# Performance work log

Hardware: AMD Instinct MI355X
Metric: run time of the kernel (lower is better)

The kernel has to match this reference:

```python
import jax, jax.numpy as jnp
import numpy as np

D_MODEL = 64
NODES = 325
TOPK = 8
HEADS = 4
D_INNER = 2 * D_MODEL      # mamba_ssm default expand=2
D_STATE = 16               # mamba_ssm default
D_CONV = 4                 # mamba_ssm default
DT_RANK = 4                # ceil(d_model/16)
B_SZ, T_LEN = 8, 64
EPS = 1e-5


def _layernorm(x, g, b):
    m = jnp.mean(x, -1, keepdims=True)
    v = jnp.mean(jnp.square(x - m), -1, keepdims=True)
    return (x - m) * jax.lax.rsqrt(v + EPS) * g + b


def _mamba(h, in_proj_w, conv_w, conv_b, x_proj_w, dt_w, dt_b, A_log, D_ssm, out_w):
    # h: (BN, T, D_MODEL)
    BN, T, _ = h.shape
    xz = h @ in_proj_w.T                      # (BN,T,2*di)
    xi, z = jnp.split(xz, 2, axis=-1)
    # depthwise causal conv1d, kernel D_CONV (unrolled: tiny fixed loop)
    xp = jnp.pad(xi, ((0, 0), (D_CONV - 1, 0), (0, 0)))
    xc = conv_b + sum(xp[:, j:j + T, :] * conv_w[:, j] for j in range(D_CONV))
    xc = jax.nn.silu(xc)
    dbl = xc @ x_proj_w.T                     # (BN,T,dt_rank+2*ds)
    dt = dbl[..., :DT_RANK]
    Bc = dbl[..., DT_RANK:DT_RANK + D_STATE]
    Cc = dbl[..., DT_RANK + D_STATE:]
    dt = jax.nn.softplus(dt @ dt_w.T + dt_b)  # (BN,T,di)
    A = -jnp.exp(A_log)                       # (di,ds)

    def step(hs, inp):
        dt_t, B_t, C_t, x_t = inp             # (BN,di),(BN,ds),(BN,ds),(BN,di)
        dA = jnp.exp(dt_t[..., None] * A)     # (BN,di,ds)
        hs = hs * dA + (dt_t * x_t)[..., None] * B_t[:, None, :]
        y = jnp.einsum('bds,bs->bd', hs, C_t)
        return hs, y

    tm = lambda a: jnp.swapaxes(a, 0, 1)      # time-major for scan
    h0 = jnp.zeros((BN, D_INNER, D_STATE), xc.dtype)
    _, ys = jax.lax.scan(step, h0, (tm(dt), tm(Bc), tm(Cc), tm(xc)))
    y = tm(ys) + D_ssm * xc
    y = y * jax.nn.silu(z)
    return y @ out_w.T


def setup_inputs() -> dict:
    key = jax.random.key(0)
    ks = jax.random.split(key, 24)
    rn = lambda k, s, sc=0.05: jax.random.normal(k, s, jnp.float32) * sc
    inp = {}
    inp['x'] = jax.random.normal(ks[0], (B_SZ, T_LEN, NODES, D_MODEL), jnp.float32)
    adj = jax.random.normal(ks[1], (NODES, NODES), jnp.float32)
    _, nbr = jax.lax.top_k(adj, TOPK)
    inp['neighbor_idx'] = nbr.astype(jnp.int32)           # (N, k) static buffer
    # temporal block
    inp['ln1_g'] = jnp.ones((D_MODEL,)); inp['ln1_b'] = jnp.zeros((D_MODEL,))
    inp['in_proj_w'] = rn(ks[2], (2 * D_INNER, D_MODEL))
    inp['conv_w'] = rn(ks[3], (D_INNER, D_CONV), 0.2)
    inp['conv_b'] = jnp.zeros((D_INNER,))
    inp['x_proj_w'] = rn(ks[4], (DT_RANK + 2 * D_STATE, D_INNER))
    inp['dt_w'] = rn(ks[5], (D_INNER, DT_RANK), 0.5)
    inp['dt_b'] = rn(ks[6], (D_INNER,), 0.5)
    inp['A_log'] = jnp.log(jnp.tile(jnp.arange(1, D_STATE + 1, dtype=jnp.float32), (D_INNER, 1)))
    inp['D_ssm'] = jnp.ones((D_INNER,))
    inp['out_w'] = rn(ks[7], (D_MODEL, D_INNER))
    # sparse graph attention
    for nm, k in (('q', 8), ('k', 9), ('v', 10), ('o', 11)):
        inp[nm + '_w'] = rn(ks[k], (D_MODEL, D_MODEL))
        inp[nm + '_b'] = jnp.zeros((D_MODEL,))
    # adaptive gate (final bias init -2.0 per module)
    inp['g1_w'] = rn(ks[12], (D_MODEL // 4, D_MODEL))
    inp['g1_b'] = jnp.zeros((D_MODEL // 4,))
    inp['g2_w'] = rn(ks[13], (1, D_MODEL // 4))
    inp['g2_b'] = jnp.full((1,), -2.0, jnp.float32)
    inp['ln2_g'] = jnp.ones((D_MODEL,)); inp['ln2_b'] = jnp.zeros((D_MODEL,))
    return inp


def reference(x, neighbor_idx, ln1_g, ln1_b, in_proj_w, conv_w, conv_b, x_proj_w,
              dt_w, dt_b, A_log, D_ssm, out_w, q_w, q_b, k_w, k_b, v_w, v_b,
              o_w, o_b, g1_w, g1_b, g2_w, g2_b, ln2_g, ln2_b):
    B, T, N, Dm = x.shape
    # --- temporal Mamba with pre-norm residual (dropout = identity, eval) ---
    xt = x.transpose(0, 2, 1, 3).reshape(B * N, T, Dm)
    xt = xt + _mamba(_layernorm(xt, ln1_g, ln1_b), in_proj_w, conv_w, conv_b,
                     x_proj_w, dt_w, dt_b, A_log, D_ssm, out_w)
    xT = xt.reshape(B, N, T, Dm).transpose(0, 2, 1, 3)     # (B,T,N,D)
    # --- sparse top-k neighbor attention ---
    hd = Dm // HEADS
    Q = (xT @ q_w.T + q_b).reshape(B, T, N, HEADS, hd)
    K = (xT @ k_w.T + k_b).reshape(B, T, N, HEADS, hd)
    V = (xT @ v_w.T + v_b).reshape(B, T, N, HEADS, hd)
    Kn = K[:, :, neighbor_idx]                 # (B,T,N,k,H,hd)
    Vn = V[:, :, neighbor_idx]
    attn = jnp.einsum('btnhd,btnkhd->btnhk', Q, Kn) * (hd ** -0.5)
    attn = jax.nn.softmax(attn, axis=-1)
    og = jnp.einsum('btnhk,btnkhd->btnhd', attn, Vn).reshape(B, T, N, Dm)
    x_graph = og @ o_w.T + o_b
    # --- adaptive gate + fusion + final norm ---
    g = jax.nn.sigmoid(jax.nn.gelu(xT @ g1_w.T + g1_b, approximate=False) @ g2_w.T + g2_b)
    out = xT + g * (x_graph - xT)
    return _layernorm(out, ln2_g, ln2_b)
```

## Files before the change

### kernel.cpp

```cpp
#include <hip/hip_runtime.h>
#include <math.h>

#define NODES   325
#define TOPK    8
#define B_SZ    8
#define T_LEN   64
#define EPS     1e-5f
#define NTOK    ((size_t)B_SZ * T_LEN * NODES)

#define WPAD    132
#define OWPAD   68
#define XCPAD   132
#define DBLPAD  40
#define OFF_H   0
#define OFF_XC  4096
#define OFF_DBL 12544
#define OFF_DTV 15104
#define OFF_W   23296
#define SMEM_BYTES ((23296+8704)*4)

__device__ __forceinline__ float waveSum64(float v){
  #pragma unroll
  for(int m=1;m<64;m<<=1) v += __shfl_xor(v, m, 64);
  return v;
}
__device__ __forceinline__ float groupSum16(float v){
  v += __shfl_xor(v, 1, 64);
  v += __shfl_xor(v, 2, 64);
  v += __shfl_xor(v, 4, 64);
  v += __shfl_xor(v, 8, 64);
  return v;
}
__device__ __forceinline__ float dot64(const float* __restrict__ s,
                                       const float* __restrict__ w, float acc){
  #pragma unroll
  for(int q=0;q<64;q++) acc = fmaf(s[q], w[q], acc);
  return acc;
}
__device__ __forceinline__ float4 f4fma(float s, float4 a, float4 acc){
  acc.x = fmaf(s, a.x, acc.x);
  acc.y = fmaf(s, a.y, acc.y);
  acc.z = fmaf(s, a.z, acc.z);
  acc.w = fmaf(s, a.w, acc.w);
  return acc;
}
__device__ __forceinline__ float dp4(float4 a, float4 b, float acc){
  acc = fmaf(a.x, b.x, acc);
  acc = fmaf(a.y, b.y, acc);
  acc = fmaf(a.z, b.z, acc);
  acc = fmaf(a.w, b.w, acc);
  return acc;
}

__global__ __launch_bounds__(512)
void opt_mamba(const float* __restrict__ x,
               const float* __restrict__ ln1_g, const float* __restrict__ ln1_b,
               const float* __restrict__ in_w,
               const float* __restrict__ conv_w, const float* __restrict__ conv_b,
               const float* __restrict__ xp_w,
               const float* __restrict__ dt_w, const float* __restrict__ dt_b,
               const float* __restrict__ A_log, const float* __restrict__ Dss,
               const float* __restrict__ out_w,
               float* __restrict__ xT)
{
  extern __shared__ float sm[];
  float* s_h   = sm + OFF_H;
  float* s_xc  = sm + OFF_XC;
  float* s_dbl = sm + OFF_DBL;
  float* s_dtv = sm + OFF_DTV;
  float* sW    = sm + OFF_W;

  const int bn   = blockIdx.x;
  const int b    = bn / NODES;
  const int n    = bn % NODES;
  const int tid  = threadIdx.x;
  const int lane = tid & 63;
  const int wv   = tid >> 6;

  const int r0 = (tid & 31) * 4;
  const int t0 = (tid >> 5) * 4;

  for(int idx = tid; idx < 128*64; idx += 512){
    int r = idx >> 6, c = idx & 63;
    sW[c*WPAD + r] = in_w[idx];
  }
  {
    const float g_ln = ln1_g[lane], b_ln = ln1_b[lane];
    #pragma unroll
    for(int i=0;i<8;i++){
      int t = wv*8 + i;
      size_t tok = (size_t)(b*T_LEN + t)*NODES + n;
      float v   = x[tok*64 + lane];
      float m   = waveSum64(v) * (1.f/64.f);
      float c   = v - m;
      float var = waveSum64(c*c) * (1.f/64.f);
      s_h[t*64 + lane] = c * rsqrtf(var + EPS) * g_ln + b_ln;
    }
  }
  __syncthreads();

  {
    float4 acc[4];
    #pragma unroll
    for(int tt=0;tt<4;tt++) acc[tt] = make_float4(0.f,0.f,0.f,0.f);
    for(int c0=0;c0<64;c0+=4){
      float4 w0 = *(const float4*)&sW[(c0+0)*WPAD + r0];
      float4 w1 = *(const float4*)&sW[(c0+1)*WPAD + r0];
      float4 w2 = *(const float4*)&sW[(c0+2)*WPAD + r0];
      float4 w3 = *(const float4*)&sW[(c0+3)*WPAD + r0];
      #pragma unroll
      for(int tt=0;tt<4;tt++){
        float4 h4 = *(const float4*)&s_h[(t0+tt)*64 + c0];
        acc[tt] = f4fma(h4.x, w0, acc[tt]);
        acc[tt] = f4fma(h4.y, w1, acc[tt]);
        acc[tt] = f4fma(h4.z, w2, acc[tt]);
        acc[tt] = f4fma(h4.w, w3, acc[tt]);
      }
    }
    #pragma unroll
    for(int tt=0;tt<4;tt++)
      *(float4*)&s_xc[(t0+tt)*XCPAD + r0] = acc[tt];
  }
  __syncthreads();

  {
    const int dd = tid & 127, tg = tid >> 7;
    float p3 = 0.f, p2 = 0.f, p1 = 0.f;
    if(tg){
      int tq = tg*16;
      p3 = s_xc[(tq-3)*XCPAD + dd];
      p2 = s_xc[(tq-2)*XCPAD + dd];
      p1 = s_xc[(tq-1)*XCPAD + dd];
    }
    __syncthreads();
    const float cw0 = conv_w[dd*4+0], cw1 = conv_w[dd*4+1];
    const float cw2 = conv_w[dd*4+2], cw3 = conv_w[dd*4+3];
    const float cb  = conv_b[dd];
    for(int t=tg*16; t<tg*16+16; t++){
      float xi = s_xc[t*XCPAD + dd];
      float v  = cb + cw0*p3 + cw1*p2 + cw2*p1 + cw3*xi;
      p3 = p2; p2 = p1; p1 = xi;
      s_xc[t*XCPAD + dd] = v / (1.f + __expf(-v));
    }
    for(int idx = tid; idx < 128*64; idx += 512){
      int r = idx >> 6, c = idx & 63;
      sW[c*WPAD + r] = in_w[128*64 + idx];
    }
  }
  __syncthreads();

  float4 zr[4];
  {
    #pragma unroll
    for(int tt=0;tt<4;tt++) zr[tt] = make_float4(0.f,0.f,0.f,0.f);
    for(int c0=0;c0<64;c0+=4){
      float4 w0 = *(const float4*)&sW[(c0+0)*WPAD + r0];
      float4 w1 = *(const float4*)&sW[(c0+1)*WPAD + r0];
      float4 w2 = *(const float4*)&sW[(c0+2)*WPAD + r0];
      float4 w3 = *(const float4*)&sW[(c0+3)*WPAD + r0];
      #pragma unroll
      for(int tt=0;tt<4;tt++){
        float4 h4 = *(const float4*)&s_h[(t0+tt)*64 + c0];
        zr[tt] = f4fma(h4.x, w0, zr[tt]);
        zr[tt] = f4fma(h4.y, w1, zr[tt]);
        zr[tt] = f4fma(h4.z, w2, zr[tt]);
        zr[tt] = f4fma(h4.w, w3, zr[tt]);
      }
    }
  }

  {
    const int td = tid & 63, rg = tid >> 6;
    const int base = rg*5;
    float dacc[5];
    #pragma unroll
    for(int i=0;i<5;i++) dacc[i] = 0.f;
    for(int c0=0;c0<128;c0+=4){
      float4 xc4 = *(const float4*)&s_xc[td*XCPAD + c0];
      #pragma unroll
      for(int i=0;i<5;i++){
        if(base+i < 36){
          float4 w4 = *(const float4*)&xp_w[(base+i)*128 + c0];
          dacc[i] = dp4(xc4, w4, dacc[i]);
        }
      }
    }
    #pragma unroll
    for(int i=0;i<5;i++)
      if(base+i < 36) s_dbl[td*DBLPAD + base + i] = dacc[i];
  }
  __syncthreads();

  {
    const int d = tid & 127, tq = tid >> 7;
    const float dtw0 = dt_w[d*4+0], dtw1 = dt_w[d*4+1];
    const float dtw2 = dt_w[d*4+2], dtw3 = dt_w[d*4+3];
    const float dtb  = dt_b[d];
    #pragma unroll
    for(int j=0;j<16;j++){
      int t = tq + j*4;
      const float* db = &s_dbl[t*DBLPAD];
      float dtv = dtb;
      dtv = fmaf(db[0], dtw0, dtv);
      dtv = fmaf(db[1], dtw1, dtv);
      dtv = fmaf(db[2], dtw2, dtv);
      dtv = fmaf(db[3], dtw3, dtv);
      dtv = fmaxf(dtv, 0.f) + log1pf(__expf(-fabsf(dtv)));
      s_dtv[t*128 + d] = dtv;
    }
  }
  __syncthreads();

  if(tid < 128){
    const int d = tid;
    float A_d[16], hs[16];
    #pragma unroll
    for(int s=0;s<16;s++){ A_d[s] = -__expf(A_log[d*16+s]); hs[s] = 0.f; }
    const float Dd = Dss[d];
    for(int t=0;t<T_LEN;t++){
      const float* db = &s_dbl[t*DBLPAD];
      float dtv = s_dtv[t*128 + d];
      float xc  = s_xc[t*XCPAD + d];
      float dx  = dtv * xc;
      float y   = 0.f;
      #pragma unroll
      for(int s=0;s<16;s++){
        float dA = __expf(dtv * A_d[s]);
        hs[s] = fmaf(dx, db[4+s], hs[s]*dA);
        y     = fmaf(hs[s], db[20+s], y);
      }
      s_xc[t*XCPAD + d] = y + Dd*xc;
    }
  }
  __syncthreads();

  {
    #pragma unroll
    for(int tt=0;tt<4;tt++){
      float4 y4 = *(const float4*)&s_xc[(t0+tt)*XCPAD + r0];
      float4 z4 = zr[tt];
      float4 u;
      u.x = y4.x * (z4.x / (1.f + __expf(-z4.x)));
      u.y = y4.y * (z4.y / (1.f + __expf(-z4.y)));
      u.z = y4.z * (z4.z / (1.f + __expf(-z4.z)));
      u.w = y4.w * (z4.w / (1.f + __expf(-z4.w)));
      *(float4*)&s_xc[(t0+tt)*XCPAD + r0] = u;
    }
    for(int idx = tid; idx < 64*128; idx += 512){
      int j = idx >> 7, c = idx & 127;
      sW[c*OWPAD + j] = out_w[idx];
    }
  }
  __syncthreads();

  {
    const int j0  = (tid & 15) * 4;
    const int t0o = (tid >> 4) * 2;
    float4 oacc[2];
    #pragma unroll
    for(int tt=0;tt<2;tt++) oacc[tt] = make_float4(0.f,0.f,0.f,0.f);
    for(int c0=0;c0<128;c0+=4){
      float4 w0 = *(const float4*)&sW[(c0+0)*OWPAD + j0];
      float4 w1 = *(const float4*)&sW[(c0+1)*OWPAD + j0];
      float4 w2 = *(const float4*)&sW[(c0+2)*OWPAD + j0];
      float4 w3 = *(const float4*)&sW[(c0+3)*OWPAD + j0];
      #pragma unroll
      for(int tt=0;tt<2;tt++){
        float4 u4 = *(const float4*)&s_xc[(t0o+tt)*XCPAD + c0];
        oacc[tt] = f4fma(u4.x, w0, oacc[tt]);
        oacc[tt] = f4fma(u4.y, w1, oacc[tt]);
        oacc[tt] = f4fma(u4.z, w2, oacc[tt]);
        oacc[tt] = f4fma(u4.w, w3, oacc[tt]);
      }
    }
    #pragma unroll
    for(int tt=0;tt<2;tt++){
      int t = t0o + tt;
      size_t tok = (size_t)(b*T_LEN + t)*NODES + n;
      float4 xv = *(const float4*)&x[tok*64 + j0];
      float4 o;
      o.x = xv.x + oacc[tt].x;
      o.y = xv.y + oacc[tt].y;
      o.z = xv.z + oacc[tt].z;
      o.w = xv.w + oacc[tt].w;
      *(float4*)&xT[tok*64 + j0] = o;
    }
  }
}

__global__ __launch_bounds__(256)
void opt_proj(const float* __restrict__ xT,
              const float* __restrict__ k_w, const float* __restrict__ k_b,
              const float* __restrict__ v_w, const float* __restrict__ v_b,
              const float* __restrict__ g1_w, const float* __restrict__ g1_b,
              const float* __restrict__ g2_w, const float* __restrict__ g2_b,
              float* __restrict__ Kb, float* __restrict__ Vb,
              float* __restrict__ gate)
{
  __shared__ float s_x[64*68];
  const int tid = threadIdx.x;
  const size_t tb = (size_t)blockIdx.x * 64;

  for(int i = tid; i < 64*64; i += 256){
    int t = i >> 6, c = i & 63;
    s_x[t*68 + c] = xT[(tb + t)*64 + c];
  }
  __syncthreads();

  const int r0 = (tid & 15) * 4;
  const int t0 = (tid >> 4) * 4;

  {
    float4 b4 = *(const float4*)&k_b[r0];
    float4 acc[4];
    #pragma unroll
    for(int tt=0;tt<4;tt++) acc[tt] = b4;
    for(int c0=0;c0<64;c0+=4){
      float4 w0 = *(const float4*)&k_w[(r0+0)*64 + c0];
      float4 w1 = *(const float4*)&k_w[(r0+1)*64 + c0];
      float4 w2 = *(const float4*)&k_w[(r0+2)*64 + c0];
      float4 w3 = *(const float4*)&k_w[(r0+3)*64 + c0];
      #pragma unroll
      for(int tt=0;tt<4;tt++){
        float4 x4 = *(const float4*)&s_x[(t0+tt)*68 + c0];
        acc[tt].x = dp4(x4, w0, acc[tt].x);
        acc[tt].y = dp4(x4, w1, acc[tt].y);
        acc[tt].z = dp4(x4, w2, acc[tt].z);
        acc[tt].w = dp4(x4, w3, acc[tt].w);
      }
    }
    #pragma unroll
    for(int tt=0;tt<4;tt++)
      *(float4*)&Kb[(tb + t0 + tt)*64 + r0] = acc[tt];
  }

  {
    float4 b4 = *(const float4*)&v_b[r0];
    float4 acc[4];
    #pragma unroll
    for(int tt=0;tt<4;tt++) acc[tt] = b4;
    for(int c0=0;c0<64;c0+=4){
      float4 w0 = *(const float4*)&v_w[(r0+0)*64 + c0];
      float4 w1 = *(const float4*)&v_w[(r0+1)*64 + c0];
      float4 w2 = *(const float4*)&v_w[(r0+2)*64 + c0];
      float4 w3 = *(const float4*)&v_w[(r0+3)*64 + c0];
      #pragma unroll
      for(int tt=0;tt<4;tt++){
        float4 x4 = *(const float4*)&s_x[(t0+tt)*68 + c0];
        acc[tt].x = dp4(x4, w0, acc[tt].x);
        acc[tt].y = dp4(x4, w1, acc[tt].y);
        acc[tt].z = dp4(x4, w2, acc[tt].z);
        acc[tt].w = dp4(x4, w3, acc[tt].w);
      }
    }
    #pragma unroll
    for(int tt=0;tt<4;tt++)
      *(float4*)&Vb[(tb + t0 + tt)*64 + r0] = acc[tt];
  }

  {
    const int td = tid >> 2;
    const int sr = (tid & 3) * 4;
    float partial = 0.f;
    #pragma unroll
    for(int i=0;i<4;i++){
      int r = sr + i;
      float u = dot64(&s_x[td*68], g1_w + r*64, g1_b[r]);
      u = 0.5f * u * (1.f + erff(u * 0.70710678118654752f));
      partial = fmaf(u, g2_w[r], partial);
    }
    partial += __shfl_xor(partial, 1, 64);
    partial += __shfl_xor(partial, 2, 64);
    if((tid & 3) == 0)
      gate[tb + td] = 1.f / (1.f + __expf(-(partial + g2_b[0])));
  }
}

__global__ __launch_bounds__(256)
void opt_attn3(const float* __restrict__ xT,
               const float* __restrict__ Kb, const float* __restrict__ Vb,
               const float* __restrict__ gate, const int* __restrict__ nbr,
               const float* __restrict__ q_w, const float* __restrict__ q_b,
               const float* __restrict__ o_w, const float* __restrict__ o_b,
               const float* __restrict__ ln2_g, const float* __restrict__ ln2_b,
               float* __restrict__ out)
{
  __shared__ float s_x[64*68];
  __shared__ float s_q[64*68];
  const int tid = threadIdx.x;
  const size_t tb = (size_t)blockIdx.x * 64;

  for(int i = tid; i < 64*64; i += 256){
    int t = i >> 6, c = i & 63;
    s_x[t*68 + c] = xT[(tb + t)*64 + c];
  }
  __syncthreads();

  {
    const int r0 = (tid & 15) * 4, t0 = (tid >> 4) * 4;
    float4 b4 = *(const float4*)&q_b[r0];
    float4 acc[4];
    #pragma unroll
    for(int tt=0;tt<4;tt++) acc[tt] = b4;
    for(int c0=0;c0<64;c0+=4){
      float4 w0 = *(const float4*)&q_w[(r0+0)*64 + c0];
      float4 w1 = *(const float4*)&q_w[(r0+1)*64 + c0];
      float4 w2 = *(const float4*)&q_w[(r0+2)*64 + c0];
      float4 w3 = *(const float4*)&q_w[(r0+3)*64 + c0];
      #pragma unroll
      for(int tt=0;tt<4;tt++){
        float4 x4 = *(const float4*)&s_x[(t0+tt)*68 + c0];
        acc[tt].x = dp4(x4, w0, acc[tt].x);
        acc[tt].y = dp4(x4, w1, acc[tt].y);
        acc[tt].z = dp4(x4, w2, acc[tt].z);
        acc[tt].w = dp4(x4, w3, acc[tt].w);
      }
    }
    #pragma unroll
    for(int tt=0;tt<4;tt++)
      *(float4*)&s_q[(t0+tt)*68 + r0] = acc[tt];
  }
  __syncthreads();

  const int td = tid >> 2, h = tid & 3;
  const size_t idxg = tb + td;
  const int n  = (int)(idxg % NODES);
  const int bt = (int)(idxg / NODES);
// ... 186 lines not shown
    float contrib = groupSum16(u * g2_w[j]);
    if(j == 0) s_gate = 1.f / (1.f + __expf(-(contrib + g2_b[0])));
  }
  __syncthreads();

  float gg = s_gate;
  float o  = xv + gg * (xg - xv);

  float mm  = waveSum64(o) * (1.f/64.f);
  float c   = o - mm;
  float var = waveSum64(c*c) * (1.f/64.f);
  out[(size_t)idx*64 + j] = c * rsqrtf(var + EPS) * ln2_g[j] + ln2_b[j];
}

extern "C" void kernel_launch(void* const* d_in, const int* in_sizes, int n_in,
                              void* d_out, int out_size, void* d_ws, size_t ws_size,
                              hipStream_t stream)
{
  const float* x      = (const float*)d_in[0];
  const int*   nbr    = (const int*  )d_in[1];
  const float* ln1_g  = (const float*)d_in[2];
  const float* ln1_b  = (const float*)d_in[3];
  const float* in_w   = (const float*)d_in[4];
  const float* conv_w = (const float*)d_in[5];
  const float* conv_b = (const float*)d_in[6];
  const float* xp_w   = (const float*)d_in[7];
  const float* dt_w   = (const float*)d_in[8];
  const float* dt_b   = (const float*)d_in[9];
  const float* A_log  = (const float*)d_in[10];
  const float* Dss    = (const float*)d_in[11];
  const float* out_w  = (const float*)d_in[12];
  const float* q_w    = (const float*)d_in[13];
  const float* q_b    = (const float*)d_in[14];
  const float* k_w    = (const float*)d_in[15];
  const float* k_b    = (const float*)d_in[16];
  const float* v_w    = (const float*)d_in[17];
  const float* v_b    = (const float*)d_in[18];
  const float* o_w    = (const float*)d_in[19];
  const float* o_b    = (const float*)d_in[20];
  const float* g1_w   = (const float*)d_in[21];
  const float* g1_b   = (const float*)d_in[22];
  const float* g2_w   = (const float*)d_in[23];
  const float* g2_b   = (const float*)d_in[24];
  const float* ln2_g  = (const float*)d_in[25];
  const float* ln2_b  = (const float*)d_in[26];

  float* xT   = (float*)d_ws;
  float* Kb   = xT + NTOK*64;
  float* Vb   = Kb + NTOK*64;
  float* gg   = Vb + NTOK*64;
  float* outp = (float*)d_out;

  const size_t need = (NTOK*64*3 + NTOK) * sizeof(float);

  (void)hipFuncSetAttribute(reinterpret_cast<const void*>(opt_mamba),
                            hipFuncAttributeMaxDynamicSharedMemorySize, SMEM_BYTES);

  opt_mamba<<<dim3(B_SZ*NODES), dim3(512), SMEM_BYTES, stream>>>(
      x, ln1_g, ln1_b, in_w, conv_w, conv_b, xp_w, dt_w, dt_b, A_log, Dss, out_w, xT);

  if(ws_size >= need){
    opt_proj<<<dim3((unsigned)(NTOK/64)), dim3(256), 0, stream>>>(
        xT, k_w, k_b, v_w, v_b, g1_w, g1_b, g2_w, g2_b, Kb, Vb, gg);
    opt_attn3<<<dim3((unsigned)(NTOK/64)), dim3(256), 0, stream>>>(
        xT, Kb, Vb, gg, nbr, q_w, q_b, o_w, o_b, ln2_g, ln2_b, outp);
  } else {
    opt_attn<<<dim3((unsigned)NTOK), dim3(64), 0, stream>>>(
        xT, nbr, q_w, q_b, k_w, k_b, v_w, v_b, o_w, o_b,
        g1_w, g1_b, g2_w, g2_b, ln2_g, ln2_b, outp);
  }
}
```

Measured before the change: 1.554 ms.

## Fuse K/V/gate projection into Mamba kernel and parallelize selective scan across threads

```diff
diff --git a/kernel.cpp b/kernel.cpp
--- a/kernel.cpp
+++ b/kernel.cpp
@@ -8,16 +8,15 @@
 #define EPS     1e-5f
 #define NTOK    ((size_t)B_SZ * T_LEN * NODES)
 
-#define WPAD    132
-#define OWPAD   68
+#define HPAD    68
 #define XCPAD   132
 #define DBLPAD  40
+#define WH      68
 #define OFF_H   0
-#define OFF_XC  4096
-#define OFF_DBL 12544
-#define OFF_DTV 15104
-#define OFF_W   23296
-#define SMEM_BYTES ((23296+8704)*4)
+#define OFF_XC  4352
+#define OFF_DBL 12800
+#define OFF_W   15360
+#define SMEM_BYTES (19712*4)
 
 __device__ __forceinline__ float waveSum64(float v){
   #pragma unroll
@@ -61,13 +60,18 @@
                const float* __restrict__ dt_w, const float* __restrict__ dt_b,
                const float* __restrict__ A_log, const float* __restrict__ Dss,
                const float* __restrict__ out_w,
-               float* __restrict__ xT)
+               const float* __restrict__ k_w, const float* __restrict__ k_b,
+               const float* __restrict__ v_w, const float* __restrict__ v_b,
+               const float* __restrict__ g1_w, const float* __restrict__ g1_b,
+               const float* __restrict__ g2_w, const float* __restrict__ g2_b,
+               float* __restrict__ xT,
+               float* __restrict__ Kb, float* __restrict__ Vb,
+               float* __restrict__ gate, int do_tail)
 {
   extern __shared__ float sm[];
   float* s_h   = sm + OFF_H;
   float* s_xc  = sm + OFF_XC;
   float* s_dbl = sm + OFF_DBL;
-  float* s_dtv = sm + OFF_DTV;
   float* sW    = sm + OFF_W;
 
   const int bn   = blockIdx.x;
@@ -77,12 +81,14 @@
   const int lane = tid & 63;
   const int wv   = tid >> 6;
 
-  const int r0 = (tid & 31) * 4;
-  const int t0 = (tid >> 5) * 4;
-
-  for(int idx = tid; idx < 128*64; idx += 512){
-    int r = idx >> 6, c = idx & 63;
-    sW[c*WPAD + r] = in_w[idx];
+  const int rA = (tid & 15) * 4;
+  const int tA = (tid >> 4) * 2;
+
+  const float4 z4 = make_float4(0.f,0.f,0.f,0.f);
+
+  for(int idx = tid; idx < 4096; idx += 512){
+    int c = idx & 63, rr = idx >> 6;
+    sW[c*WH + rr] = in_w[rr*64 + c];
   }
   {
     const float g_ln = ln1_g[lane], b_ln = ln1_b[lane];
@@ -94,32 +100,47 @@
       float m   = waveSum64(v) * (1.f/64.f);
       float c   = v - m;
       float var = waveSum64(c*c) * (1.f/64.f);
-      s_h[t*64 + lane] = c * rsqrtf(var + EPS) * g_ln + b_ln;
-    }
-  }
-  __syncthreads();
-
-  {
-    float4 acc[4];
-    #pragma unroll
-    for(int tt=0;tt<4;tt++) acc[tt] = make_float4(0.f,0.f,0.f,0.f);
-    for(int c0=0;c0<64;c0+=4){
-      float4 w0 = *(const float4*)&sW[(c0+0)*WPAD + r0];
-      float4 w1 = *(const float4*)&sW[(c0+1)*WPAD + r0];
-      float4 w2 = *(const float4*)&sW[(c0+2)*WPAD + r0];
-      float4 w3 = *(const float4*)&sW[(c0+3)*WPAD + r0];
-      #pragma unroll
-      for(int tt=0;tt<4;tt++){
-        float4 h4 = *(const float4*)&s_h[(t0+tt)*64 + c0];
-        acc[tt] = f4fma(h4.x, w0, acc[tt]);
-        acc[tt] = f4fma(h4.y, w1, acc[tt]);
-        acc[tt] = f4fma(h4.z, w2, acc[tt]);
-        acc[tt] = f4fma(h4.w, w3, acc[tt]);
-      }
-    }
-    #pragma unroll
-    for(int tt=0;tt<4;tt++)
-      *(float4*)&s_xc[(t0+tt)*XCPAD + r0] = acc[tt];
+      s_h[t*HPAD + lane] = c * rsqrtf(var + EPS) * g_ln + b_ln;
+    }
+  }
+  __syncthreads();
+
+  {
+    float4 a0 = z4, a1 = z4;
+    for(int c0=0;c0<64;c0+=4){
+      float4 w0 = *(const float4*)&sW[(c0+0)*WH + rA];
+      float4 w1 = *(const float4*)&sW[(c0+1)*WH + rA];
+      float4 w2 = *(const float4*)&sW[(c0+2)*WH + rA];
+      float4 w3 = *(const float4*)&sW[(c0+3)*WH + rA];
+      float4 h0 = *(const float4*)&s_h[(tA+0)*HPAD + c0];
+      float4 h1 = *(const float4*)&s_h[(tA+1)*HPAD + c0];
+      a0 = f4fma(h0.x,w0,a0); a0 = f4fma(h0.y,w1,a0); a0 = f4fma(h0.z,w2,a0); a0 = f4fma(h0.w,w3,a0);
+      a1 = f4fma(h1.x,w0,a1); a1 = f4fma(h1.y,w1,a1); a1 = f4fma(h1.z,w2,a1); a1 = f4fma(h1.w,w3,a1);
+    }
+    *(float4*)&s_xc[(tA+0)*XCPAD + rA] = a0;
+    *(float4*)&s_xc[(tA+1)*XCPAD + rA] = a1;
+  }
+  __syncthreads();
+  for(int idx = tid; idx < 4096; idx += 512){
+    int c = idx & 63, rr = idx >> 6;
+    sW[c*WH + rr] = in_w[(64+rr)*64 + c];
+  }
+  __syncthreads();
+
+  {
+    float4 a0 = z4, a1 = z4;
+    for(int c0=0;c0<64;c0+=4){
+      float4 w0 = *(const float4*)&sW[(c0+0)*WH + rA];
+      float4 w1 = *(const float4*)&sW[(c0+1)*WH + rA];
+      float4 w2 = *(const float4*)&sW[(c0+2)*WH + rA];
+      float4 w3 = *(const float4*)&sW[(c0+3)*WH + rA];
+      float4 h0 = *(const float4*)&s_h[(tA+0)*HPAD + c0];
+      float4 h1 = *(const float4*)&s_h[(tA+1)*HPAD + c0];
+      a0 = f4fma(h0.x,w0,a0); a0 = f4fma(h0.y,w1,a0); a0 = f4fma(h0.z,w2,a0); a0 = f4fma(h0.w,w3,a0);
+      a1 = f4fma(h1.x,w0,a1); a1 = f4fma(h1.y,w1,a1); a1 = f4fma(h1.z,w2,a1); a1 = f4fma(h1.w,w3,a1);
+    }
+    *(float4*)&s_xc[(tA+0)*XCPAD + 64 + rA] = a0;
+    *(float4*)&s_xc[(tA+1)*XCPAD + 64 + rA] = a1;
   }
   __syncthreads();
 
@@ -142,31 +163,48 @@
       p3 = p2; p2 = p1; p1 = xi;
       s_xc[t*XCPAD + dd] = v / (1.f + __expf(-v));
     }
-    for(int idx = tid; idx < 128*64; idx += 512){
-      int r = idx >> 6, c = idx & 63;
-      sW[c*WPAD + r] = in_w[128*64 + idx];
-    }
-  }
-  __syncthreads();
-
-  float4 zr[4];
-  {
-    #pragma unroll
-    for(int tt=0;tt<4;tt++) zr[tt] = make_float4(0.f,0.f,0.f,0.f);
-    for(int c0=0;c0<64;c0+=4){
-      float4 w0 = *(const float4*)&sW[(c0+0)*WPAD + r0];
-      float4 w1 = *(const float4*)&sW[(c0+1)*WPAD + r0];
-      float4 w2 = *(const float4*)&sW[(c0+2)*WPAD + r0];
-      float4 w3 = *(const float4*)&sW[(c0+3)*WPAD + r0];
-      #pragma unroll
-      for(int tt=0;tt<4;tt++){
-        float4 h4 = *(const float4*)&s_h[(t0+tt)*64 + c0];
-        zr[tt] = f4fma(h4.x, w0, zr[tt]);
-        zr[tt] = f4fma(h4.y, w1, zr[tt]);
-        zr[tt] = f4fma(h4.z, w2, zr[tt]);
-        zr[tt] = f4fma(h4.w, w3, zr[tt]);
-      }
-    }
+    for(int idx = tid; idx < 4096; idx += 512){
+      int c = idx & 63, rr = idx >> 6;
+      sW[c*WH + rr] = in_w[(128+rr)*64 + c];
+    }
+  }
+  __syncthreads();
+
+  float4 zrA[2], zrB[2];
+  {
+    float4 a0 = z4, a1 = z4;
+    for(int c0=0;c0<64;c0+=4){
+      float4 w0 = *(const float4*)&sW[(c0+0)*WH + rA];
+      float4 w1 = *(const float4*)&sW[(c0+1)*WH + rA];
+      float4 w2 = *(const float4*)&sW[(c0+2)*WH + rA];
+      float4 w3 = *(const float4*)&sW[(c0+3)*WH + rA];
+      float4 h0 = *(const float4*)&s_h[(tA+0)*HPAD + c0];
+      float4 h1 = *(const float4*)&s_h[(tA+1)*HPAD + c0];
+      a0 = f4fma(h0.x,w0,a0); a0 = f4fma(h0.y,w1,a0); a0 = f4fma(h0.z,w2,a0); a0 = f4fma(h0.w,w3,a0);
+      a1 = f4fma(h1.x,w0,a1); a1 = f4fma(h1.y,w1,a1); a1 = f4fma(h1.z,w2,a1); a1 = f4fma(h1.w,w3,a1);
+    }
+    zrA[0] = a0; zrA[1] = a1;
+  }
+  __syncthreads();
+  for(int idx = tid; idx < 4096; idx += 512){
+    int c = idx & 63, rr = idx >> 6;
+    sW[c*WH + rr] = in_w[(192+rr)*64 + c];
+  }
+  __syncthreads();
+
+  {
+    float4 a0 = z4, a1 = z4;
+    for(int c0=0;c0<64;c0+=4){
+      float4 w0 = *(const float4*)&sW[(c0+0)*WH + rA];
+      float4 w1 = *(const float4*)&sW[(c0+1)*WH + rA];
+      float4 w2 = *(const float4*)&sW[(c0+2)*WH + rA];
+      float4 w3 = *(const float4*)&sW[(c0+3)*WH + rA];
+      float4 h0 = *(const float4*)&s_h[(tA+0)*HPAD + c0];
+      float4 h1 = *(const float4*)&s_h[(tA+1)*HPAD + c0];
+      a0 = f4fma(h0.x,w0,a0); a0 = f4fma(h0.y,w1,a0); a0 = f4fma(h0.z,w2,a0); a0 = f4fma(h0.w,w3,a0);
+      a1 = f4fma(h1.x,w0,a1); a1 = f4fma(h1.y,w1,a1); a1 = f4fma(h1.z,w2,a1); a1 = f4fma(h1.w,w3,a1);
+    }
+    zrB[0] = a0; zrB[1] = a1;
   }
 
   {
@@ -192,187 +230,155 @@
   __syncthreads();
 
   {
-    const int d = tid & 127, tq = tid >> 7;
+    const int d  = tid >> 2;
+    const int sq = tid & 3;
+    float A_d[4], hs[4];
+    #pragma unroll
+    for(int i=0;i<4;i++){ A_d[i] = -__expf(A_log[d*16 + sq*4 + i]); hs[i] = 0.f; }
     const float dtw0 = dt_w[d*4+0], dtw1 = dt_w[d*4+1];
     const float dtw2 = dt_w[d*4+2], dtw3 = dt_w[d*4+3];
-    const float dtb  = dt_b[d];
-    #pragma unroll
-    for(int j=0;j<16;j++){
-      int t = tq + j*4;
-      const float* db = &s_dbl[t*DBLPAD];
-      float dtv = dtb;
-      dtv = fmaf(db[0], dtw0, dtv);
-      dtv = fmaf(db[1], dtw1, dtv);
-      dtv = fmaf(db[2], dtw2, dtv);
-      dtv = fmaf(db[3], dtw3, dtv);
-      dtv = fmaxf(dtv, 0.f) + log1pf(__expf(-fabsf(dtv)));
-      s_dtv[t*128 + d] = dtv;
-    }
-  }
-  __syncthreads();
-
-  if(tid < 128){
-    const int d = tid;
-    float A_d[16], hs[16];
-    #pragma unroll
-    for(int s=0;s<16;s++){ A_d[s] = -__expf(A_log[d*16+s]); hs[s] = 0.f; }
-    const float Dd = Dss[d];
+    const float dtb  = dt_b[d], Dd = Dss[d];
+    #pragma unroll 2
     for(int t=0;t<T_LEN;t++){
       const float* db = &s_dbl[t*DBLPAD];
-      float dtv = s_dtv[t*128 + d];
-      float xc  = s_xc[t*XCPAD + d];
-      float dx  = dtv * xc;
-      float y   = 0.f;
+      float4 dt4 = *(const float4*)db;
+      float dtv = dtb;
+      dtv = fmaf(dt4.x, dtw0, dtv);
+      dtv = fmaf(dt4.y, dtw1, dtv);
+      dtv = fmaf(dt4.z, dtw2, dtv);
+      dtv = fmaf(dt4.w, dtw3, dtv);
+      dtv = fmaxf(dtv, 0.f) + log1pf(__expf(-fabsf(dtv)));
+      float xc = s_xc[t*XCPAD + d];
+      float dx = dtv * xc;
+      float4 Bv = *(const float4*)&db[4  + sq*4];
+      float4 Cv = *(const float4*)&db[20 + sq*4];
+      float yp = 0.f;
+      hs[0] = fmaf(dx, Bv.x, hs[0]*__expf(dtv*A_d[0])); yp = fmaf(hs[0], Cv.x, yp);
+      hs[1] = fmaf(dx, Bv.y, hs[1]*__expf(dtv*A_d[1])); yp = fmaf(hs[1], Cv.y, yp);
+      hs[2] = fmaf(dx, Bv.z, hs[2]*__expf(dtv*A_d[2])); yp = fmaf(hs[2], Cv.z, yp);
+      hs[3] = fmaf(dx, Bv.w, hs[3]*__expf(dtv*A_d[3])); yp = fmaf(hs[3], Cv.w, yp);
+      yp += __shfl_xor(yp, 1, 64);
+      yp += __shfl_xor(yp, 2, 64);
+      if(sq == 0) s_xc[t*XCPAD + d] = yp + Dd*xc;
+    }
+  }
+  __syncthreads();
+
+  {
+    #pragma unroll
+    for(int tt=0;tt<2;tt++){
+      float4 y4 = *(const float4*)&s_xc[(tA+tt)*XCPAD + rA];
+      float4 zv = zrA[tt];
+      float4 u;
+      u.x = y4.x * (zv.x / (1.f + __expf(-zv.x)));
+      u.y = y4.y * (zv.y / (1.f + __expf(-zv.y)));
+      u.z = y4.z * (zv.z / (1.f + __expf(-zv.z)));
+      u.w = y4.w * (zv.w / (1.f + __expf(-zv.w)));
+      *(float4*)&s_xc[(tA+tt)*XCPAD + rA] = u;
+      y4 = *(const float4*)&s_xc[(tA+tt)*XCPAD + 64 + rA];
+      zv = zrB[tt];
+      u.x = y4.x * (zv.x / (1.f + __expf(-zv.x)));
+      u.y = y4.y * (zv.y / (1.f + __expf(-zv.y)));
+      u.z = y4.z * (zv.z / (1.f + __expf(-zv.z)));
+      u.w = y4.w * (zv.w / (1.f + __expf(-zv.w)));
+      *(float4*)&s_xc[(tA+tt)*XCPAD + 64 + rA] = u;
+    }
+    for(int idx = tid; idx < 4096; idx += 512){
+      int c = idx & 63, j = idx >> 6;
+      sW[c*WH + j] = out_w[j*128 + c];
+    }
+  }
+  __syncthreads();
+
+  {
+    float4 a0 = z4, a1 = z4;
+    for(int c0=0;c0<64;c0+=4){
+      float4 w0 = *(const float4*)&sW[(c0+0)*WH + rA];
+      float4 w1 = *(const float4*)&sW[(c0+1)*WH + rA];
+      float4 w2 = *(const float4*)&sW[(c0+2)*WH + rA];
+      float4 w3 = *(const float4*)&sW[(c0+3)*WH + rA];
+      float4 u0 = *(const float4*)&s_xc[(tA+0)*XCPAD + c0];
+      float4 u1 = *(const float4*)&s_xc[(tA+1)*XCPAD + c0];
+      a0 = f4fma(u0.x,w0,a0); a0 = f4fma(u0.y,w1,a0); a0 = f4fma(u0.z,w2,a0); a0 = f4fma(u0.w,w3,a0);
+      a1 = f4fma(u1.x,w0,a1); a1 = f4fma(u1.y,w1,a1); a1 = f4fma(u1.z,w2,a1); a1 = f4fma(u1.w,w3,a1);
+    }
+    __syncthreads();
+    for(int idx = tid; idx < 4096; idx += 512){
+      int c = idx & 63, j = idx >> 6;
+      sW[c*WH + j] = out_w[j*128 + 64 + c];
+    }
+    __syncthreads();
+    for(int c0=0;c0<64;c0+=4){
+      float4 w0 = *(const float4*)&sW[(c0+0)*WH + rA];
+      float4 w1 = *(const float4*)&sW[(c0+1)*WH + rA];
+      float4 w2 = *(const float4*)&sW[(c0+2)*WH + rA];
+      float4 w3 = *(const float4*)&sW[(c0+3)*WH + rA];
+      float4 u0 = *(const float4*)&s_xc[(tA+0)*XCPAD + 64 + c0];
+      float4 u1 = *(const float4*)&s_xc[(tA+1)*XCPAD + 64 + c0];
+      a0 = f4fma(u0.x,w0,a0); a0 = f4fma(u0.y,w1,a0); a0 = f4fma(u0.z,w2,a0); a0 = f4fma(u0.w,w3,a0);
+      a1 = f4fma(u1.x,w0,a1); a1 = f4fma(u1.y,w1,a1); a1 = f4fma(u1.z,w2,a1); a1 = f4fma(u1.w,w3,a1);
+    }
+    #pragma unroll
+    for(int tt=0;tt<2;tt++){
+      float4 a = (tt==0) ? a0 : a1;
+      int t = tA + tt;
+      size_t tok = (size_t)(b*T_LEN + t)*NODES + n;
+      float4 xv = *(const float4*)&x[tok*64 + rA];
+      float4 o;
+      o.x = xv.x + a.x; o.y = xv.y + a.y; o.z = xv.z + a.z; o.w = xv.w + a.w;
+      *(float4*)&xT[tok*64 + rA] = o;
+      *(float4*)&s_h[t*HPAD + rA] = o;
+    }
+  }
+
+  if(do_tail){
+    __syncthreads();
+    {
+      float4 kb4 = *(const float4*)&k_b[rA];
+      float4 vb4 = *(const float4*)&v_b[rA];
+      float4 ka0 = kb4, ka1 = kb4, va0 = vb4, va1 = vb4;
+      for(int c0=0;c0<64;c0+=4){
+        float4 x0 = *(const float4*)&s_h[(tA+0)*HPAD + c0];
+        float4 x1 = *(const float4*)&s_h[(tA+1)*HPAD + c0];
+        float4 w0 = *(const float4*)&k_w[(rA+0)*64 + c0];
+        float4 w1 = *(const float4*)&k_w[(rA+1)*64 + c0];
+        float4 w2 = *(const float4*)&k_w[(rA+2)*64 + c0];
+        float4 w3 = *(const float4*)&k_w[(rA+3)*64 + c0];
+        ka0.x = dp4(x0,w0,ka0.x); ka0.y = dp4(x0,w1,ka0.y); ka0.z = dp4(x0,w2,ka0.z); ka0.w = dp4(x0,w3,ka0.w);
+        ka1.x = dp4(x1,w0,ka1.x); ka1.y = dp4(x1,w1,ka1.y); ka1.z = dp4(x1,w2,ka1.z); ka1.w = dp4(x1,w3,ka1.w);
+        w0 = *(const float4*)&v_w[(rA+0)*64 + c0];
+        w1 = *(const float4*)&v_w[(rA+1)*64 + c0];
+        w2 = *(const float4*)&v_w[(rA+2)*64 + c0];
+        w3 = *(const float4*)&v_w[(rA+3)*64 + c0];
+        va0.x = dp4(x0,w0,va0.x); va0.y = dp4(x0,w1,va0.y); va0.z = dp4(x0,w2,va0.z); va0.w = dp4(x0,w3,va0.w);
+        va1.x = dp4(x1,w0,va1.x); va1.y = dp4(x1,w1,va1.y); va1.z = dp4(x1,w2,va1.z); va1.w = dp4(x1,w3,va1.w);
+      }
+      size_t tok0 = (size_t)(b*T_LEN + tA+0)*NODES + n;
+      size_t tok1 = (size_t)(b*T_LEN + tA+1)*NODES + n;
+      *(float4*)&Kb[tok0*64 + rA] = ka0;
+      *(float4*)&Kb[tok1*64 + rA] = ka1;
+      *(float4*)&Vb[tok0*64 + rA] = va0;
+      *(float4*)&Vb[tok1*64 + rA] = va1;
+    }
+    {
+      const int td = tid >> 3;
+      const int sr = (tid & 7) * 2;
+      float partial = 0.f;
       #pragma unroll
-      for(int s=0;s<16;s++){
-        float dA = __expf(dtv * A_d[s]);
-        hs[s] = fmaf(dx, db[4+s], hs[s]*dA);
-        y     = fmaf(hs[s], db[20+s], y);
+      for(int i=0;i<2;i++){
+        int r = sr + i;
+        float u = dot64(&s_h[td*HPAD], g1_w + r*64, g1_b[r]);
+        u = 0.5f * u * (1.f + erff(u * 0.70710678118654752f));
+        partial = fmaf(u, g2_w[r], partial);
       }
-      s_xc[t*XCPAD + d] = y + Dd*xc;
-    }
-  }
-  __syncthreads();
-
-  {
-    #pragma unroll
-    for(int tt=0;tt<4;tt++){
-      float4 y4 = *(const float4*)&s_xc[(t0+tt)*XCPAD + r0];
-      float4 z4 = zr[tt];
-      float4 u;
-      u.x = y4.x * (z4.x / (1.f + __expf(-z4.x)));
-      u.y = y4.y * (z4.y / (1.f + __expf(-z4.y)));
-      u.z = y4.z * (z4.z / (1.f + __expf(-z4.z)));
-      u.w = y4.w * (z4.w / (1.f + __expf(-z4.w)));
-      *(float4*)&s_xc[(t0+tt)*XCPAD + r0] = u;
-    }
-    for(int idx = tid; idx < 64*128; idx += 512){
-      int j = idx >> 7, c = idx & 127;
-      sW[c*OWPAD + j] = out_w[idx];
-    }
-  }
-  __syncthreads();
-
-  {
-    const int j0  = (tid & 15) * 4;
-    const int t0o = (tid >> 4) * 2;
-    float4 oacc[2];
-    #pragma unroll
-    for(int tt=0;tt<2;tt++) oacc[tt] = make_float4(0.f,0.f,0.f,0.f);
-    for(int c0=0;c0<128;c0+=4){
-      float4 w0 = *(const float4*)&sW[(c0+0)*OWPAD + j0];
-      float4 w1 = *(const float4*)&sW[(c0+1)*OWPAD + j0];
-      float4 w2 = *(const float4*)&sW[(c0+2)*OWPAD + j0];
-      float4 w3 = *(const float4*)&sW[(c0+3)*OWPAD + j0];
-      #pragma unroll
-      for(int tt=0;tt<2;tt++){
-        float4 u4 = *(const float4*)&s_xc[(t0o+tt)*XCPAD + c0];
-        oacc[tt] = f4fma(u4.x, w0, oacc[tt]);
-        oacc[tt] = f4fma(u4.y, w1, oacc[tt]);
-        oacc[tt] = f4fma(u4.z, w2, oacc[tt]);
-        oacc[tt] = f4fma(u4.w, w3, oacc[tt]);
+      partial += __shfl_xor(partial, 1, 64);
+      partial += __shfl_xor(partial, 2, 64);
+      partial += __shfl_xor(partial, 4, 64);
+      if((tid & 7) == 0){
+        size_t tok = (size_t)(b*T_LEN + td)*NODES + n;
+        gate[tok] = 1.f / (1.f + __expf(-(partial + g2_b[0])));
       }
     }
-    #pragma unroll
-    for(int tt=0;tt<2;tt++){
-      int t = t0o + tt;
-      size_t tok = (size_t)(b*T_LEN + t)*NODES + n;
-      float4 xv = *(const float4*)&x[tok*64 + j0];
-      float4 o;
-      o.x = xv.x + oacc[tt].x;
-      o.y = xv.y + oacc[tt].y;
-      o.z = xv.z + oacc[tt].z;
-      o.w = xv.w + oacc[tt].w;
-      *(float4*)&xT[tok*64 + j0] = o;
-    }
-  }
-}
-
-__global__ __launch_bounds__(256)
-void opt_proj(const float* __restrict__ xT,
-              const float* __restrict__ k_w, const float* __restrict__ k_b,
-              const float* __restrict__ v_w, const float* __restrict__ v_b,
-              const float* __restrict__ g1_w, const float* __restrict__ g1_b,
-              const float* __restrict__ g2_w, const float* __restrict__ g2_b,
-              float* __restrict__ Kb, float* __restrict__ Vb,
-              float* __restrict__ gate)
-{
-  __shared__ float s_x[64*68];
-  const int tid = threadIdx.x;
-  const size_t tb = (size_t)blockIdx.x * 64;
-
-  for(int i = tid; i < 64*64; i += 256){
-    int t = i >> 6, c = i & 63;
-    s_x[t*68 + c] = xT[(tb + t)*64 + c];
-  }
-  __syncthreads();
-
-  const int r0 = (tid & 15) * 4;
-  const int t0 = (tid >> 4) * 4;
-
-  {
-    float4 b4 = *(const float4*)&k_b[r0];
-    float4 acc[4];
-    #pragma unroll
-    for(int tt=0;tt<4;tt++) acc[tt] = b4;
-    for(int c0=0;c0<64;c0+=4){
-      float4 w0 = *(const float4*)&k_w[(r0+0)*64 + c0];
-      float4 w1 = *(const float4*)&k_w[(r0+1)*64 + c0];
-      float4 w2 = *(const float4*)&k_w[(r0+2)*64 + c0];
-      float4 w3 = *(const float4*)&k_w[(r0+3)*64 + c0];
-      #pragma unroll
-      for(int tt=0;tt<4;tt++){
-        float4 x4 = *(const float4*)&s_x[(t0+tt)*68 + c0];
-        acc[tt].x = dp4(x4, w0, acc[tt].x);
-        acc[tt].y = dp4(x4, w1, acc[tt].y);
-        acc[tt].z = dp4(x4, w2, acc[tt].z);
-        acc[tt].w = dp4(x4, w3, acc[tt].w);
-      }
-    }
-    #pragma unroll
-    for(int tt=0;tt<4;tt++)
-      *(float4*)&Kb[(tb + t0 + tt)*64 + r0] = acc[tt];
-  }
-
-  {
-    float4 b4 = *(const float4*)&v_b[r0];
-    float4 acc[4];
-    #pragma unroll
-    for(int tt=0;tt<4;tt++) acc[tt] = b4;
-    for(int c0=0;c0<64;c0+=4){
-      float4 w0 = *(const float4*)&v_w[(r0+0)*64 + c0];
-      float4 w1 = *(const float4*)&v_w[(r0+1)*64 + c0];
-      float4 w2 = *(const float4*)&v_w[(r0+2)*64 + c0];
-      float4 w3 = *(const float4*)&v_w[(r0+3)*64 + c0];
-      #pragma unroll
-      for(int tt=0;tt<4;tt++){
-        float4 x4 = *(const float4*)&s_x[(t0+tt)*68 + c0];
-        acc[tt].x = dp4(x4, w0, acc[tt].x);
-        acc[tt].y = dp4(x4, w1, acc[tt].y);
-        acc[tt].z = dp4(x4, w2, acc[tt].z);
-        acc[tt].w = dp4(x4, w3, acc[tt].w);
-      }
-    }
-    #pragma unroll
-    for(int tt=0;tt<4;tt++)
-      *(float4*)&Vb[(tb + t0 + tt)*64 + r0] = acc[tt];
-  }
-
-  {
-    const int td = tid >> 2;
-    const int sr = (tid & 3) * 4;
-    float partial = 0.f;
-    #pragma unroll
-    for(int i=0;i<4;i++){
-      int r = sr + i;
-      float u = dot64(&s_x[td*68], g1_w + r*64, g1_b[r]);
-      u = 0.5f * u * (1.f + erff(u * 0.70710678118654752f));
-      partial = fmaf(u, g2_w[r], partial);
-    }
-    partial += __shfl_xor(partial, 1, 64);
-    partial += __shfl_xor(partial, 2, 64);
-    if((tid & 3) == 0)
-      gate[tb + td] = 1.f / (1.f + __expf(-(partial + g2_b[0])));
   }
 }
 
@@ -665,16 +671,17 @@
   float* outp = (float*)d_out;
 
   const size_t need = (NTOK*64*3 + NTOK) * sizeof(float);
+  const int tail = (ws_size >= need) ? 1 : 0;
 
   (void)hipFuncSetAttribute(reinterpret_cast<const void*>(opt_mamba),
                             hipFuncAttributeMaxDynamicSharedMemorySize, SMEM_BYTES);
 
   opt_mamba<<<dim3(B_SZ*NODES), dim3(512), SMEM_BYTES, stream>>>(
-      x, ln1_g, ln1_b, in_w, conv_w, conv_b, xp_w, dt_w, dt_b, A_log, Dss, out_w, xT);
-
-  if(ws_size >= need){
-    opt_proj<<<dim3((unsigned)(NTOK/64)), dim3(256), 0, stream>>>(
-        xT, k_w, k_b, v_w, v_b, g1_w, g1_b, g2_w, g2_b, Kb, Vb, gg);
+      x, ln1_g, ln1_b, in_w, conv_w, conv_b, xp_w, dt_w, dt_b, A_log, Dss, out_w,
+      k_w, k_b, v_w, v_b, g1_w, g1_b, g2_w, g2_b,
+      xT, Kb, Vb, gg, tail);
+
+  if(tail){
     opt_attn3<<<dim3((unsigned)(NTOK/64)), dim3(256), 0, stream>>>(
         xT, Kb, Vb, gg, nbr, q_w, q_b, o_w, o_b, ln2_g, ln2_b, outp);
   } else {
```

Result: slower. 1.910 ms (+22.9%).

## Read Mamba weights from global/L2, shrink LDS, and split scan across 4 lanes per channel

Applied to the files above, without the earlier changes.

```diff
diff --git a/kernel.cpp b/kernel.cpp
--- a/kernel.cpp
+++ b/kernel.cpp
@@ -8,16 +8,13 @@
 #define EPS     1e-5f
 #define NTOK    ((size_t)B_SZ * T_LEN * NODES)
 
-#define WPAD    132
-#define OWPAD   68
+#define HPAD    68
 #define XCPAD   132
 #define DBLPAD  40
 #define OFF_H   0
-#define OFF_XC  4096
-#define OFF_DBL 12544
-#define OFF_DTV 15104
-#define OFF_W   23296
-#define SMEM_BYTES ((23296+8704)*4)
+#define OFF_XC  4352
+#define OFF_DBL 12800
+#define SMEM_BYTES (15360*4)
 
 __device__ __forceinline__ float waveSum64(float v){
   #pragma unroll
@@ -52,7 +49,7 @@
   return acc;
 }
 
-__global__ __launch_bounds__(512)
+__global__ __launch_bounds__(512, 4)
 void opt_mamba(const float* __restrict__ x,
                const float* __restrict__ ln1_g, const float* __restrict__ ln1_b,
                const float* __restrict__ in_w,
@@ -67,8 +64,6 @@
   float* s_h   = sm + OFF_H;
   float* s_xc  = sm + OFF_XC;
   float* s_dbl = sm + OFF_DBL;
-  float* s_dtv = sm + OFF_DTV;
-  float* sW    = sm + OFF_W;
 
   const int bn   = blockIdx.x;
   const int b    = bn / NODES;
@@ -77,13 +72,8 @@
   const int lane = tid & 63;
   const int wv   = tid >> 6;
 
-  const int r0 = (tid & 31) * 4;
-  const int t0 = (tid >> 5) * 4;
-
-  for(int idx = tid; idx < 128*64; idx += 512){
-    int r = idx >> 6, c = idx & 63;
-    sW[c*WPAD + r] = in_w[idx];
-  }
+  const float4 zero4 = make_float4(0.f,0.f,0.f,0.f);
+
   {
     const float g_ln = ln1_g[lane], b_ln = ln1_b[lane];
     #pragma unroll
@@ -94,32 +84,35 @@
       float m   = waveSum64(v) * (1.f/64.f);
       float c   = v - m;
       float var = waveSum64(c*c) * (1.f/64.f);
-      s_h[t*64 + lane] = c * rsqrtf(var + EPS) * g_ln + b_ln;
-    }
-  }
-  __syncthreads();
-
-  {
-    float4 acc[4];
-    #pragma unroll
-    for(int tt=0;tt<4;tt++) acc[tt] = make_float4(0.f,0.f,0.f,0.f);
+      s_h[t*HPAD + lane] = c * rsqrtf(var + EPS) * g_ln + b_ln;
+    }
+  }
+  __syncthreads();
+
+  const int rA = (tid & 31) * 4;
+  const int tB = (tid >> 5) * 4;
+
+  {
+    float4 a[4];
+    #pragma unroll
+    for(int tt=0;tt<4;tt++) a[tt] = zero4;
     for(int c0=0;c0<64;c0+=4){
-      float4 w0 = *(const float4*)&sW[(c0+0)*WPAD + r0];
-      float4 w1 = *(const float4*)&sW[(c0+1)*WPAD + r0];
-      float4 w2 = *(const float4*)&sW[(c0+2)*WPAD + r0];
-      float4 w3 = *(const float4*)&sW[(c0+3)*WPAD + r0];
+      float4 w0 = *(const float4*)&in_w[(rA+0)*64 + c0];
+      float4 w1 = *(const float4*)&in_w[(rA+1)*64 + c0];
+      float4 w2 = *(const float4*)&in_w[(rA+2)*64 + c0];
+      float4 w3 = *(const float4*)&in_w[(rA+3)*64 + c0];
       #pragma unroll
       for(int tt=0;tt<4;tt++){
-        float4 h4 = *(const float4*)&s_h[(t0+tt)*64 + c0];
-        acc[tt] = f4fma(h4.x, w0, acc[tt]);
-        acc[tt] = f4fma(h4.y, w1, acc[tt]);
-        acc[tt] = f4fma(h4.z, w2, acc[tt]);
-        acc[tt] = f4fma(h4.w, w3, acc[tt]);
+        float4 h4 = *(const float4*)&s_h[(tB+tt)*HPAD + c0];
+        a[tt].x = dp4(h4, w0, a[tt].x);
+        a[tt].y = dp4(h4, w1, a[tt].y);
+        a[tt].z = dp4(h4, w2, a[tt].z);
+        a[tt].w = dp4(h4, w3, a[tt].w);
       }
     }
     #pragma unroll
     for(int tt=0;tt<4;tt++)
-      *(float4*)&s_xc[(t0+tt)*XCPAD + r0] = acc[tt];
+      *(float4*)&s_xc[(tB+tt)*XCPAD + rA] = a[tt];
   }
   __syncthreads();
 
@@ -142,29 +135,25 @@
       p3 = p2; p2 = p1; p1 = xi;
       s_xc[t*XCPAD + dd] = v / (1.f + __expf(-v));
     }
-    for(int idx = tid; idx < 128*64; idx += 512){
-      int r = idx >> 6, c = idx & 63;
-      sW[c*WPAD + r] = in_w[128*64 + idx];
-    }
   }
   __syncthreads();
 
   float4 zr[4];
   {
     #pragma unroll
-    for(int tt=0;tt<4;tt++) zr[tt] = make_float4(0.f,0.f,0.f,0.f);
+    for(int tt=0;tt<4;tt++) zr[tt] = zero4;
     for(int c0=0;c0<64;c0+=4){
-      float4 w0 = *(const float4*)&sW[(c0+0)*WPAD + r0];
-      float4 w1 = *(const float4*)&sW[(c0+1)*WPAD + r0];
-      float4 w2 = *(const float4*)&sW[(c0+2)*WPAD + r0];
-      float4 w3 = *(const float4*)&sW[(c0+3)*WPAD + r0];
+      float4 w0 = *(const float4*)&in_w[(128+rA+0)*64 + c0];
+      float4 w1 = *(const float4*)&in_w[(128+rA+1)*64 + c0];
+      float4 w2 = *(const float4*)&in_w[(128+rA+2)*64 + c0];
+      float4 w3 = *(const float4*)&in_w[(128+rA+3)*64 + c0];
       #pragma unroll
       for(int tt=0;tt<4;tt++){
-        float4 h4 = *(const float4*)&s_h[(t0+tt)*64 + c0];
-        zr[tt] = f4fma(h4.x, w0, zr[tt]);
-        zr[tt] = f4fma(h4.y, w1, zr[tt]);
-        zr[tt] = f4fma(h4.z, w2, zr[tt]);
-        zr[tt] = f4fma(h4.w, w3, zr[tt]);
+        float4 h4 = *(const float4*)&s_h[(tB+tt)*HPAD + c0];
+        zr[tt].x = dp4(h4, w0, zr[tt].x);
+        zr[tt].y = dp4(h4, w1, zr[tt].y);
+        zr[tt].z = dp4(h4, w2, zr[tt].z);
+        zr[tt].w = dp4(h4, w3, zr[tt].w);
       }
     }
   }
@@ -192,44 +181,35 @@
   __syncthreads();
 
   {
-    const int d = tid & 127, tq = tid >> 7;
+    const int d  = tid >> 2;
+    const int sq = tid & 3;
+    float A_d[4], hs[4];
+    #pragma unroll
+    for(int i=0;i<4;i++){ A_d[i] = -__expf(A_log[d*16 + sq*4 + i]); hs[i] = 0.f; }
     const float dtw0 = dt_w[d*4+0], dtw1 = dt_w[d*4+1];
     const float dtw2 = dt_w[d*4+2], dtw3 = dt_w[d*4+3];
-    const float dtb  = dt_b[d];
-    #pragma unroll
-    for(int j=0;j<16;j++){
-      int t = tq + j*4;
-      const float* db = &s_dbl[t*DBLPAD];
-      float dtv = dtb;
-      dtv = fmaf(db[0], dtw0, dtv);
-      dtv = fmaf(db[1], dtw1, dtv);
-      dtv = fmaf(db[2], dtw2, dtv);
-      dtv = fmaf(db[3], dtw3, dtv);
-      dtv = fmaxf(dtv, 0.f) + log1pf(__expf(-fabsf(dtv)));
-      s_dtv[t*128 + d] = dtv;
-    }
-  }
-  __syncthreads();
-
-  if(tid < 128){
-    const int d = tid;
-    float A_d[16], hs[16];
-    #pragma unroll
-    for(int s=0;s<16;s++){ A_d[s] = -__expf(A_log[d*16+s]); hs[s] = 0.f; }
-    const float Dd = Dss[d];
+    const float dtb  = dt_b[d], Dd = Dss[d];
     for(int t=0;t<T_LEN;t++){
       const float* db = &s_dbl[t*DBLPAD];
-      float dtv = s_dtv[t*128 + d];
-      float xc  = s_xc[t*XCPAD + d];
-      float dx  = dtv * xc;
-      float y   = 0.f;
-      #pragma unroll
-      for(int s=0;s<16;s++){
-        float dA = __expf(dtv * A_d[s]);
-        hs[s] = fmaf(dx, db[4+s], hs[s]*dA);
-        y     = fmaf(hs[s], db[20+s], y);
-      }
-      s_xc[t*XCPAD + d] = y + Dd*xc;
+      float4 dt4 = *(const float4*)db;
+      float dtv = dtb;
+      dtv = fmaf(dt4.x, dtw0, dtv);
+      dtv = fmaf(dt4.y, dtw1, dtv);
+      dtv = fmaf(dt4.z, dtw2, dtv);
+      dtv = fmaf(dt4.w, dtw3, dtv);
+      dtv = fmaxf(dtv, 0.f) + log1pf(__expf(-fabsf(dtv)));
+      float xc = s_xc[t*XCPAD + d];
+      float dx = dtv * xc;
+      float4 Bv = *(const float4*)&db[4  + sq*4];
+      float4 Cv = *(const float4*)&db[20 + sq*4];
+      float yp = 0.f;
+      hs[0] = fmaf(dx, Bv.x, hs[0]*__expf(dtv*A_d[0])); yp = fmaf(hs[0], Cv.x, yp);
+      hs[1] = fmaf(dx, Bv.y, hs[1]*__expf(dtv*A_d[1])); yp = fmaf(hs[1], Cv.y, yp);
+      hs[2] = fmaf(dx, Bv.z, hs[2]*__expf(dtv*A_d[2])); yp = fmaf(hs[2], Cv.z, yp);
+      hs[3] = fmaf(dx, Bv.w, hs[3]*__expf(dtv*A_d[3])); yp = fmaf(hs[3], Cv.w, yp);
+      yp += __shfl_xor(yp, 1, 64);
+      yp += __shfl_xor(yp, 2, 64);
+      if(sq == 0) s_xc[t*XCPAD + d] = yp + Dd*xc;
     }
   }
   __syncthreads();
@@ -237,53 +217,41 @@
   {
     #pragma unroll
     for(int tt=0;tt<4;tt++){
-      float4 y4 = *(const float4*)&s_xc[(t0+tt)*XCPAD + r0];
-      float4 z4 = zr[tt];
+      float4 y4 = *(const float4*)&s_xc[(tB+tt)*XCPAD + rA];
+      float4 zv = zr[tt];
       float4 u;
-      u.x = y4.x * (z4.x / (1.f + __expf(-z4.x)));
-      u.y = y4.y * (z4.y / (1.f + __expf(-z4.y)));
-      u.z = y4.z * (z4.z / (1.f + __expf(-z4.z)));
-      u.w = y4.w * (z4.w / (1.f + __expf(-z4.w)));
-      *(float4*)&s_xc[(t0+tt)*XCPAD + r0] = u;
-    }
-    for(int idx = tid; idx < 64*128; idx += 512){
-      int j = idx >> 7, c = idx & 127;
-      sW[c*OWPAD + j] = out_w[idx];
-    }
-  }
-  __syncthreads();
-
-  {
-    const int j0  = (tid & 15) * 4;
-    const int t0o = (tid >> 4) * 2;
-    float4 oacc[2];
-    #pragma unroll
-    for(int tt=0;tt<2;tt++) oacc[tt] = make_float4(0.f,0.f,0.f,0.f);
+      u.x = y4.x * (zv.x / (1.f + __expf(-zv.x)));
+      u.y = y4.y * (zv.y / (1.f + __expf(-zv.y)));
+      u.z = y4.z * (zv.z / (1.f + __expf(-zv.z)));
+      u.w = y4.w * (zv.w / (1.f + __expf(-zv.w)));
+      *(float4*)&s_xc[(tB+tt)*XCPAD + rA] = u;
+    }
+  }
+  __syncthreads();
+
+  {
+    const int rO = (tid & 15) * 4;
+    const int tO = (tid >> 4) * 2;
+    float4 a0 = zero4, a1 = zero4;
     for(int c0=0;c0<128;c0+=4){
-      float4 w0 = *(const float4*)&sW[(c0+0)*OWPAD + j0];
-      float4 w1 = *(const float4*)&sW[(c0+1)*OWPAD + j0];
-      float4 w2 = *(const float4*)&sW[(c0+2)*OWPAD + j0];
-      float4 w3 = *(const float4*)&sW[(c0+3)*OWPAD + j0];
-      #pragma unroll
-      for(int tt=0;tt<2;tt++){
-        float4 u4 = *(const float4*)&s_xc[(t0o+tt)*XCPAD + c0];
-        oacc[tt] = f4fma(u4.x, w0, oacc[tt]);
-        oacc[tt] = f4fma(u4.y, w1, oacc[tt]);
-        oacc[tt] = f4fma(u4.z, w2, oacc[tt]);
-        oacc[tt] = f4fma(u4.w, w3, oacc[tt]);
-      }
+      float4 w0 = *(const float4*)&out_w[(rO+0)*128 + c0];
+      float4 w1 = *(const float4*)&out_w[(rO+1)*128 + c0];
+      float4 w2 = *(const float4*)&out_w[(rO+2)*128 + c0];
+      float4 w3 = *(const float4*)&out_w[(rO+3)*128 + c0];
+      float4 u0 = *(const float4*)&s_xc[(tO+0)*XCPAD + c0];
+      float4 u1 = *(const float4*)&s_xc[(tO+1)*XCPAD + c0];
+      a0.x = dp4(u0,w0,a0.x); a0.y = dp4(u0,w1,a0.y); a0.z = dp4(u0,w2,a0.z); a0.w = dp4(u0,w3,a0.w);
+      a1.x = dp4(u1,w0,a1.x); a1.y = dp4(u1,w1,a1.y); a1.z = dp4(u1,w2,a1.z); a1.w = dp4(u1,w3,a1.w);
     }
     #pragma unroll
     for(int tt=0;tt<2;tt++){
-      int t = t0o + tt;
+      float4 a = (tt==0) ? a0 : a1;
+      int t = tO + tt;
       size_t tok = (size_t)(b*T_LEN + t)*NODES + n;
-      float4 xv = *(const float4*)&x[tok*64 + j0];
+      float4 xv = *(const float4*)&x[tok*64 + rO];
       float4 o;
-      o.x = xv.x + oacc[tt].x;
-      o.y = xv.y + oacc[tt].y;
-      o.z = xv.z + oacc[tt].z;
-      o.w = xv.w + oacc[tt].w;
-      *(float4*)&xT[tok*64 + j0] = o;
+      o.x = xv.x + a.x; o.y = xv.y + a.y; o.z = xv.z + a.z; o.w = xv.w + a.w;
+      *(float4*)&xT[tok*64 + rO] = o;
     }
   }
 }
```

After: 2.661 ms. 71.2% more time.
